# Kernel tuning notes

Measured on AMD Instinct MI355X. Metric: run time of the kernel, lower is better.

## Reference

```python
import jax, jax.numpy as jnp
import numpy as np

B, P, C, WIN = 64, 24, 40, 64          # batch, acoustic params, phoneme classes, window
L1 = WIN - 4                            # after conv k=5: 60
L2 = L1 - 4                             # after primary conv k=5: 56
R = P * L2                              # num_routes = 24*56 = 1344
IC, OC = 32, 16                         # capsule in/out channels
NUM_ITERS = 3


def squash(x, axis=-1):
    sq = jnp.sum(x * x, axis=axis, keepdims=True)
    return (sq / (1.0 + sq)) * x / (jnp.sqrt(sq) + 1e-8)


def conv1d(x, w, b):
    # x: (B, Cin, L), w: (Cout, Cin, K)
    out = jax.lax.conv_general_dilated(x, w, (1,), 'VALID',
                                       dimension_numbers=('NCH', 'OIH', 'NCH'))
    return out + b[None, :, None]


def batchnorm(x, g, b):
    # training-mode BN over (batch, length) per channel; x: (B, Ch, L)
    m = jnp.mean(x, axis=(0, 2), keepdims=True)
    v = jnp.var(x, axis=(0, 2), keepdims=True)
    return g[None, :, None] * (x - m) / jnp.sqrt(v + 1e-5) + b[None, :, None]


def setup_inputs() -> dict:
    key = jax.random.key(0)
    ks = jax.random.split(key, 12)
    d = {}
    d['x'] = jax.random.normal(ks[0], (B, WIN, P), dtype=jnp.float32)
    # project: Conv1d(24 -> 256, k=5) + BN(256)
    d['conv1_w'] = jax.random.normal(ks[1], (256, P, 5), dtype=jnp.float32) * (1.0 / np.sqrt(P * 5))
    d['conv1_b'] = jnp.zeros((256,), dtype=jnp.float32)
    d['bn1_g'] = jnp.ones((256,), dtype=jnp.float32)
    d['bn1_b'] = jnp.zeros((256,), dtype=jnp.float32)
    d['prim_w'] = jax.random.normal(ks[2], (P * 32, 256, 5), dtype=jnp.float32) * (1.0 / np.sqrt(256 * 5))
    d['prim_b'] = jnp.zeros((P * 32,), dtype=jnp.float32)
    d['bn2_g'] = jnp.ones((32,), dtype=jnp.float32)
    d['bn2_b'] = jnp.zeros((32,), dtype=jnp.float32)
    # digit capsule routing weights (1, C, R, 16, 32) as in torch (randn)
    d['W_cap'] = jax.random.normal(ks[3], (1, C, R, OC, IC), dtype=jnp.float32) * 0.05
    # classifier: Linear(16*C -> 256), Linear(256 -> C)
    d['cls_w1'] = jax.random.normal(ks[4], (256, OC * C), dtype=jnp.float32) * (1.0 / np.sqrt(OC * C))
    d['cls_b1'] = jnp.zeros((256,), dtype=jnp.float32)
    d['cls_w2'] = jax.random.normal(ks[5], (C, 256), dtype=jnp.float32) * (1.0 / np.sqrt(256))
    d['cls_b2'] = jnp.zeros((C,), dtype=jnp.float32)
    d['dec_w1'] = jax.random.normal(ks[6], (256, OC * C), dtype=jnp.float32) * (1.0 / np.sqrt(OC * C))
    d['dec_b1'] = jnp.zeros((256,), dtype=jnp.float32)
    d['dec_w2'] = jax.random.normal(ks[7], (WIN * P, 256), dtype=jnp.float32) * (1.0 / np.sqrt(256))
    d['dec_b2'] = jnp.zeros((WIN * P,), dtype=jnp.float32)
    return d


def reference(x, conv1_w, conv1_b, bn1_g, bn1_b, prim_w, prim_b, bn2_g, bn2_b,
              W_cap, cls_w1, cls_b1, cls_w2, cls_b2, dec_w1, dec_b1, dec_w2, dec_b2):
    h = jax.nn.relu(batchnorm(conv1d(jnp.transpose(x, (0, 2, 1)), conv1_w, conv1_b), bn1_g, bn1_b))
    # primary capsules: fused conv -> (B, 24*32, 56); capsule i occupies length slice i
    u = conv1d(h, prim_w, prim_b)                       # (B, 768, 56)
    u = u.reshape(B, P, 32, L2).transpose(0, 2, 1, 3).reshape(B, 32, R)  # concat along length dim
    u = batchnorm(u, bn2_g, bn2_b)
    u = squash(jnp.transpose(u, (0, 2, 1)), axis=-1)    # (B, R, 32)
    # digit capsule: u_hat = W @ x  -> (B, C, R, 16)
    u_hat = jnp.einsum('crdi,bri->bcrd', W_cap[0], u)
    # dynamic routing
    b_ij = jnp.zeros((B, C, R, 1), dtype=u_hat.dtype)
    for it in range(NUM_ITERS):
        c_ij = jax.nn.softmax(b_ij, axis=1)             # softmax over capsules
        s_j = jnp.sum(c_ij * u_hat, axis=2)             # (B, C, 16)
        v_j = squash(s_j, axis=-1)
        if it < NUM_ITERS - 1:
            a_ij = jnp.einsum('bcrd,bcd->bcr', u_hat, v_j)[..., None]
            b_ij = b_ij + a_ij
    flat = v_j.reshape(B, -1)                           # (B, 640)
    logits = jax.nn.relu(flat @ cls_w1.T + cls_b1) @ cls_w2.T + cls_b2
    pred_y = jax.nn.softmax(logits, axis=-1)
    # y is None branch: one-hot of argmax
    y = jax.nn.one_hot(jnp.argmax(pred_y, axis=1), C, dtype=v_j.dtype)
    masked = (v_j * y[:, :, None]).reshape(B, -1)
    pred_x = jax.nn.sigmoid(jax.nn.relu(masked @ dec_w1.T + dec_b1) @ dec_w2.T + dec_b2)
    pred_x = pred_x.reshape(B, WIN, P)
    return (pred_x, pred_y)
```

## Files before the change

### kernel.cpp

```cpp
#include <hip/hip_runtime.h>
#include <math.h>

#define BB_ 64
#define P_  24
#define C_  40
#define WIN_ 64
#define L1_ 60
#define L2_ 56
#define R_  1344

#define O_USQ   0ull
#define O_UHAT  2752512ull
#define O_H     30277632ull
#define O_HB    3735552ull
#define O_WT    4227072ull
#define O_UP    25755648ull
#define O_HID   31260672ull
#define O_HD    31277056ull
#define O_STATS 57802752ull
#define O_A1    57803328ull
#define O_B1S   57803584ull
#define O_A2    57803840ull
#define O_B2S   57803872ull
#define O_S     57803904ull
#define O_V     57967744ull
#define WS_FLOATS_NEEDED 58008704ull

typedef short bf16x8 __attribute__((ext_vector_type(8)));
typedef float f32x4 __attribute__((ext_vector_type(4)));

__device__ __forceinline__ float dot4f(float4 a, float4 b) {
    return a.x*b.x + a.y*b.y + a.z*b.z + a.w*b.w;
}

__device__ __forceinline__ unsigned short f2bf(float x) {
    unsigned int u = __float_as_uint(x);
    u += 0x7fffu + ((u >> 16) & 1u);
    return (unsigned short)(u >> 16);
}
__device__ __forceinline__ float bfl(unsigned int u) {
    return __uint_as_float(u << 16);
}
__device__ __forceinline__ float bfh(unsigned int u) {
    return __uint_as_float(u & 0xffff0000u);
}

__global__ void k0w(const float* __restrict__ w2, unsigned short* __restrict__ wt) {
    int o2 = blockIdx.x, t = threadIdx.x;
    const float* src = &w2[(size_t)o2 * 1280 + t * 5];
    #pragma unroll
    for (int kt = 0; kt < 5; kt++)
        wt[((size_t)kt * 768 + o2) * 256 + t] = f2bf(src[kt]);
}

__global__ void k1_conv1(const float* __restrict__ x, const float* __restrict__ w1,
                         const float* __restrict__ c1b, float* __restrict__ h) {
    __shared__ float xs[24 * 20];
    __shared__ float wl[64 * 121];
    int t = threadIdx.x;
    int lq = blockIdx.x, b = blockIdx.y, ocg = blockIdx.z;
    for (int idx = t; idx < 456; idx += 256) {
        int p = idx / 19, tau = idx - p * 19;
        xs[p * 20 + tau] = x[b * 1536 + (lq * 15 + tau) * 24 + p];
    }
    for (int idx = t; idx < 7680; idx += 256) {
        int o_ = idx / 120, cix = idx - o_ * 120;
        wl[o_ * 121 + cix] = w1[(ocg * 64 + o_) * 120 + cix];
    }
    __syncthreads();
    int g = t >> 6;
    int ol = t & 63;
    int LV = (g < 3) ? 4 : 3;
    int o = ocg * 64 + ol;
    float acc[4] = {0.f, 0.f, 0.f, 0.f};
    for (int p = 0; p < 24; p++) {
        float4 xa = *(const float4*)&xs[p * 20 + g * 4];
        float4 xb = *(const float4*)&xs[p * 20 + g * 4 + 4];
        float xr[8] = {xa.x, xa.y, xa.z, xa.w, xb.x, xb.y, xb.z, xb.w};
        #pragma unroll
        for (int k = 0; k < 5; k++) {
            float w = wl[ol * 121 + p * 5 + k];
            #pragma unroll
            for (int li = 0; li < 4; li++) acc[li] += xr[li + k] * w;
        }
    }
    for (int li = 0; li < LV; li++) {
        int l = lq * 15 + g * 4 + li;
        h[(size_t)(b * 60 + l) * 256 + o] = acc[li] + c1b[o];
    }
}

__global__ void k2a(const float* __restrict__ h, float* __restrict__ sum1, float* __restrict__ ss1) {
    int t = threadIdx.x;
    float s = 0.f, q = 0.f;
    for (int i = 0; i < 64; i++) {
        float v = h[(size_t)(blockIdx.x * 64 + i) * 256 + t];
        s += v; q += v * v;
    }
    atomicAdd(&sum1[t], s);
    atomicAdd(&ss1[t], q);
}

__global__ void k2b(const float* __restrict__ sum1, const float* __restrict__ ss1,
                    const float* __restrict__ g, const float* __restrict__ be,
                    float* __restrict__ a1, float* __restrict__ b1s) {
    int o = threadIdx.x;
    float m = sum1[o] * (1.f / 3840.f);
    float v = ss1[o] * (1.f / 3840.f) - m * m;
    float a = g[o] / sqrtf(v + 1e-5f);
    a1[o] = a;
    b1s[o] = be[o] - m * a;
}

__global__ void k2c(const float* __restrict__ h, const float* __restrict__ a1,
                    const float* __restrict__ b1s, unsigned short* __restrict__ hb) {
    int gid = blockIdx.x * 256 + threadIdx.x;
    int base = gid * 4;
    int ic = base & 255;
    float4 v = *(const float4*)&h[base];
    float4 a = *(const float4*)&a1[ic];
    float4 bb = *(const float4*)&b1s[ic];
    unsigned int w0 = (unsigned int)f2bf(fmaxf(v.x * a.x + bb.x, 0.f))
                    | ((unsigned int)f2bf(fmaxf(v.y * a.y + bb.y, 0.f)) << 16);
    unsigned int w1 = (unsigned int)f2bf(fmaxf(v.z * a.z + bb.z, 0.f))
                    | ((unsigned int)f2bf(fmaxf(v.w * a.w + bb.w, 0.f)) << 16);
    uint2 o = {w0, w1};
    *(uint2*)&hb[base] = o;
}

__global__ __launch_bounds__(256) void k3_mfma(
        const unsigned short* __restrict__ hb, const unsigned short* __restrict__ wt,
        const float* __restrict__ pb, float* __restrict__ up) {
    __shared__ unsigned short hs[68 * 40];
    __shared__ unsigned short wsd[5 * 64 * 40];
    int t = threadIdx.x;
    int m0 = blockIdx.x * 64;
    int b = blockIdx.y;
    int wid = t >> 6, lane = t & 63;
    int wm = wid >> 1, wn = wid & 1;
    int ln = lane & 15, grp = lane >> 4;

    f32x4 acc[2][2];
    #pragma unroll
    for (int i = 0; i < 2; i++)
        #pragma unroll
        for (int j = 0; j < 2; j++) acc[i][j] = (f32x4){0.f, 0.f, 0.f, 0.f};

    for (int ic0 = 0; ic0 < 256; ic0 += 32) {
        __syncthreads();
        for (int idx = t; idx < 272; idx += 256) {
            int row = idx >> 2, q = idx & 3;
            int hrow = row < 60 ? row : 59;
            uint4 v = *(const uint4*)&hb[((size_t)b * 60 + hrow) * 256 + ic0 + q * 8];
            *(uint4*)&hs[row * 40 + q * 8] = v;
        }
        #pragma unroll
        for (int it = 0; it < 5; it++) {
            int idx = it * 256 + t;
            int row = idx >> 2, q = idx & 3;
            int kt = row >> 6, o2l = row & 63;
            uint4 v = *(const uint4*)&wt[((size_t)kt * 768 + m0 + o2l) * 256 + ic0 + q * 8];
            *(uint4*)&wsd[row * 40 + q * 8] = v;
        }
        __syncthreads();
        #pragma unroll
        for (int kt = 0; kt < 5; kt++) {
            bf16x8 af0 = *(const bf16x8*)&wsd[(kt * 64 + wm * 32 + ln) * 40 + grp * 8];
            bf16x8 af1 = *(const bf16x8*)&wsd[(kt * 64 + wm * 32 + 16 + ln) * 40 + grp * 8];
            bf16x8 bf0 = *(const bf16x8*)&hs[(wn * 32 + ln + kt) * 40 + grp * 8];
            bf16x8 bf1 = *(const bf16x8*)&hs[(wn * 32 + 16 + ln + kt) * 40 + grp * 8];
            acc[0][0] = __builtin_amdgcn_mfma_f32_16x16x32_bf16(af0, bf0, acc[0][0], 0, 0, 0);
            acc[0][1] = __builtin_amdgcn_mfma_f32_16x16x32_bf16(af0, bf1, acc[0][1], 0, 0, 0);
            acc[1][0] = __builtin_amdgcn_mfma_f32_16x16x32_bf16(af1, bf0, acc[1][0], 0, 0, 0);
            acc[1][1] = __builtin_amdgcn_mfma_f32_16x16x32_bf16(af1, bf1, acc[1][1], 0, 0, 0);
        }
    }
    #pragma unroll
    for (int ms = 0; ms < 2; ms++) {
        int o2 = m0 + wm * 32 + ms * 16 + grp * 4;
        float4 pv = *(const float4*)&pb[o2];
        #pragma unroll
        for (int ns = 0; ns < 2; ns++) {
            int l = wn * 32 + ns * 16 + ln;
            if (l < 56) {
                float4 v;
                v.x = acc[ms][ns][0] + pv.x;
                v.y = acc[ms][ns][1] + pv.y;
                v.z = acc[ms][ns][2] + pv.z;
                v.w = acc[ms][ns][3] + pv.w;
                *(float4*)&up[(size_t)b * 43008 + (size_t)l * 768 + o2] = v;
            }
        }
    }
}

__global__ void k4s(const float* __restrict__ up, float* __restrict__ sum2, float* __restrict__ ss2) {
    __shared__ float rs[256], rq[256];
    int t = threadIdx.x;
    float s = 0.f, q = 0.f;
    for (int i = 0; i < 32; i++) {
        size_t row = (size_t)(blockIdx.x * 32 + i) * 768;
        for (int c0 = 0; c0 < 768; c0 += 256) {
            float v = up[row + c0 + t];
            s += v; q += v * v;
        }
    }
    rs[t] = s; rq[t] = q;
    __syncthreads();
    if (t < 32) {
        float S = 0.f, Q = 0.f;
        for (int g2 = 0; g2 < 8; g2++) { S += rs[t + 32 * g2]; Q += rq[t + 32 * g2]; }
        atomicAdd(&sum2[t], S);
        atomicAdd(&ss2[t], Q);
    }
}

__global__ void k4b(const float* __restrict__ sum2, const float* __restrict__ ss2,
                    const float* __restrict__ g, const float* __restrict__ be,
                    float* __restrict__ a2, float* __restrict__ b2s) {
    int j = threadIdx.x;
    if (j >= 32) return;
    float m = sum2[j] * (1.f / 86016.f);
    float v = ss2[j] * (1.f / 86016.f) - m * m;
    float a = g[j] / sqrtf(v + 1e-5f);
    a2[j] = a;
    b2s[j] = be[j] - m * a;
}

__global__ void k5(const float* __restrict__ up, const float* __restrict__ a2,
                   const float* __restrict__ b2s, float* __restrict__ usq) {
    int t = threadIdx.x;
    int row = blockIdx.x * 8 + (t >> 5);
    int j = t & 31;
    int b = row / 1344, r = row - b * 1344;
    int p = r / 56, l = r - p * 56;
    float v = up[(size_t)b * 43008 + (size_t)l * 768 + p * 32 + j];
    float xv = a2[j] * v + b2s[j];
    float sq = xv * xv;
    #pragma unroll
    for (int m = 16; m >= 1; m >>= 1) sq += __shfl_xor(sq, m, 32);
    float scale = (sq / (1.f + sq)) / (sqrtf(sq) + 1e-8f);
    usq[(size_t)row * 32 + j] = xv * scale;
}

__global__ __launch_bounds__(256) void k6_mfma(const float* __restrict__ usq,
                                               const float* __restrict__ W,
                                               unsigned short* __restrict__ uhb) {
    __shared__ unsigned short ub[64 * 40];
    __shared__ unsigned short db[2][4 * 64 * 20];
    int t = threadIdx.x;
    int r = blockIdx.x;
    {
        int b = t >> 2, ch = t & 3;
        const float* src = &usq[((size_t)b * 1344 + r) * 32 + ch * 8];
        float4 v0 = *(const float4*)&src[0];
        float4 v1 = *(const float4*)&src[4];
        uint4 pk;
        pk.x = (unsigned)f2bf(v0.x) | ((unsigned)f2bf(v0.y) << 16);
        pk.y = (unsigned)f2bf(v0.z) | ((unsigned)f2bf(v0.w) << 16);
        pk.z = (unsigned)f2bf(v1.x) | ((unsigned)f2bf(v1.y) << 16);
        pk.w = (unsigned)f2bf(v1.z) | ((unsigned)f2bf(v1.w) << 16);
        *(uint4*)&ub[b * 40 + ch * 8] = pk;
    }
    __syncthreads();
    int w = t >> 6, lane = t & 63;
    int ln = lane & 15, g = lane >> 4;
    bf16x8 bfr[4];
    #pragma unroll
    for (int nt = 0; nt < 4; nt++)
        bfr[nt] = *(const bf16x8*)&ub[(nt * 16 + ln) * 40 + g * 8];

    const float* abase = &W[((size_t)w * 1344 + r) * 512 + (size_t)ln * 32 + g * 8];
    float4 c0 = *(const float4*)&abase[0];
    float4 c1 = *(const float4*)&abase[4];
    for (int j = 0; j < 10; j++) {
        float4 n0, n1;
        if (j < 9) {
            const float* nsrc = abase + (size_t)(j + 1) * 4 * 688128ull;
            n0 = *(const float4*)&nsrc[0];
            n1 = *(const float4*)&nsrc[4];
        }
        union { bf16x8 v; unsigned int u[4]; } af;
        af.u[0] = (unsigned)f2bf(c0.x) | ((unsigned)f2bf(c0.y) << 16);
        af.u[1] = (unsigned)f2bf(c0.z) | ((unsigned)f2bf(c0.w) << 16);
        af.u[2] = (unsigned)f2bf(c1.x) | ((unsigned)f2bf(c1.y) << 16);
        af.u[3] = (unsigned)f2bf(c1.z) | ((unsigned)f2bf(c1.w) << 16);
        unsigned short* dbj = db[j & 1];
        #pragma unroll
        for (int nt = 0; nt < 4; nt++) {
            f32x4 acc = (f32x4){0.f, 0.f, 0.f, 0.f};
            acc = __builtin_amdgcn_mfma_f32_16x16x32_bf16(af.v, bfr[nt], acc, 0, 0, 0);
            int b = nt * 16 + ln;
            unsigned lo = (unsigned)f2bf(acc[0]) | ((unsigned)f2bf(acc[1]) << 16);
            unsigned hi = (unsigned)f2bf(acc[2]) | ((unsigned)f2bf(acc[3]) << 16);
            uint2 o = {lo, hi};
            *(uint2*)&dbj[(w * 64 + b) * 20 + g * 4] = o;
        }
        __syncthreads();
        {
            int b2 = t >> 2, q = t & 3;
            const unsigned short* srcl = &dbj[(q * 64 + b2) * 20];
            uint4 x0 = *(const uint4*)&srcl[0];
            uint4 x1 = *(const uint4*)&srcl[8];
            unsigned short* dst = &uhb[(((size_t)b2 * 1344 + r) * 40 + j * 4 + q) * 16];
            *(uint4*)&dst[0] = x0;
            *(uint4*)&dst[8] = x1;
        }
        c0 = n0; c1 = n1;
    }
}

template<int UNIFORM>
__global__ void k_route(const unsigned short* __restrict__ uhb, const float* __restrict__ vsum,
                        float* __restrict__ spart) {
    __shared__ float sl[2560];
    int t = threadIdx.x, wid = t >> 6, lane = t & 63;
    int b = blockIdx.y, rt = blockIdx.x;
    bool act = lane < 40;
    int c = act ? lane : 0;
    float4 vs0 = {0,0,0,0}, vs1 = vs0, vs2 = vs0, vs3 = vs0;
    if (UNIFORM == 0 && act) {
        const float4* vp = (const float4*)&vsum[b * 640 + c * 16];
        vs0 = vp[0]; vs1 = vp[1]; vs2 = vp[2]; vs3 = vp[3];
    }
    float4 ac0 = {0,0,0,0}, ac1 = ac0, ac2 = ac0, ac3 = ac0;
    for (int i = 0; i < 8; i++) {
        int r = rt * 32 + wid * 8 + i;
        const uint4* u4 = (const uint4*)&uhb[((size_t)(b * 1344 + r) * 40 + c) * 16];
        float4 a0 = {0,0,0,0}, a1 = a0, a2 = a0, a3 = a0;
        if (act) {
            uint4 q0 = u4[0], q1 = u4[1];
            a0.x = bfl(q0.x); a0.y = bfh(q0.x); a0.z = bfl(q0.y); a0.w = bfh(q0.y);
            a1.x = bfl(q0.z); a1.y = bfh(q0.z); a1.z = bfl(q0.w); a1.w = bfh(q0.w);
            a2.x = bfl(q1.x); a2.y = bfh(q1.x); a2.z = bfl(q1.y); a2.w = bfh(q1.y);
            a3.x = bfl(q1.z); a3.y = bfh(q1.z); a3.z = bfl(q1.w); a3.w = bfh(q1.w);
        }
        float w;
        if (UNIFORM) {
            w = 0.025f;
        } else {
            float dt = act ? (dot4f(a0, vs0) + dot4f(a1, vs1) + dot4f(a2, vs2) + dot4f(a3, vs3))
                           : -1e30f;
            float mx = dt;
            #pragma unroll
            for (int m2 = 32; m2 >= 1; m2 >>= 1) mx = fmaxf(mx, __shfl_xor(mx, m2));
            float e = act ? __expf(dt - mx) : 0.f;
            float se = e;
            #pragma unroll
            for (int m2 = 32; m2 >= 1; m2 >>= 1) se += __shfl_xor(se, m2);
            w = e / se;
        }
        ac0.x += w * a0.x; ac0.y += w * a0.y; ac0.z += w * a0.z; ac0.w += w * a0.w;
        ac1.x += w * a1.x; ac1.y += w * a1.y; ac1.z += w * a1.z; ac1.w += w * a1.w;
        ac2.x += w * a2.x; ac2.y += w * a2.y; ac2.z += w * a2.z; ac2.w += w * a2.w;
        ac3.x += w * a3.x; ac3.y += w * a3.y; ac3.z += w * a3.z; ac3.w += w * a3.w;
    }
    if (act) {
        float4* sp = (float4*)&sl[wid * 640 + c * 16];
        sp[0] = ac0; sp[1] = ac1; sp[2] = ac2; sp[3] = ac3;
    }
    __syncthreads();
    float* dst = spart + ((size_t)rt * 64 + b) * 640;
    for (int jj = t; jj < 640; jj += 256)
        dst[jj] = sl[jj] + sl[640 + jj] + sl[1280 + jj] + sl[1920 + jj];
}

__global__ void k8(const float* __restrict__ sp, float* __restrict__ vout,
                   float* __restrict__ vsum, int addsum) {
    int t = threadIdx.x;
    int row = blockIdx.x * 16 + (t >> 4);
    int d = t & 15;
    int b = row / 40, c = row - b * 40;
    const float* p = sp + (size_t)b * 640 + c * 16 + d;
    float v = 0.f;
    #pragma unroll 6
    for (int rt = 0; rt < 42; rt++) v += p[(size_t)rt * 40960];
    float sq = v * v;
    #pragma unroll
    for (int m = 8; m >= 1; m >>= 1) sq += __shfl_xor(sq, m, 16);
    float scale = (sq / (1.f + sq)) / (sqrtf(sq) + 1e-8f);
    float o = v * scale;
    vout[row * 16 + d] = o;
    if (addsum) vsum[row * 16 + d] += o;
}

__global__ void k10a(const float* __restrict__ v, const float* __restrict__ cw1,
                     const float* __restrict__ cb1, float* __restrict__ hid) {
    __shared__ float flat[640];
    int t = threadIdx.x;
    int b = blockIdx.x, hq = blockIdx.y;
    for (int j = t; j < 640; j += 256) flat[j] = v[b * 640 + j];
    __syncthreads();
    int h_l = t >> 2, s = t & 3;
    int h = hq * 64 + h_l;
    const float4* wr = (const float4*)&cw1[(size_t)h * 640 + s * 160];
    float a = 0.f;
    #pragma unroll
    for (int u = 0; u < 40; u++) {
        float4 w4 = wr[u];
        float4 f4 = *(const float4*)&flat[s * 160 + u * 4];
        a += dot4f(w4, f4);
    }
    a += __shfl_xor(a, 1);
    a += __shfl_xor(a, 2);
    if (s == 0) hid[b * 256 + h] = fmaxf(a + cb1[h], 0.f);
}

__global__ void k10bc(const float* __restrict__ v, const float* __restrict__ hid,
                      const float* __restrict__ cw2, const float* __restrict__ cb2,
                      const float* __restrict__ dw1, const float* __restrict__ db1,
                      float* __restrict__ out, float* __restrict__ hd) {
    __shared__ float hl[256], lgs[40], msk[16];
    __shared__ float smx, ssum;
    __shared__ int chat;
    int t = threadIdx.x, b = blockIdx.x;
    if (t < 256) hl[t] = hid[b * 256 + t];
    __syncthreads();
    {
        int c = t >> 3, s = t & 7;
        float p = 0.f;
        const float4* w4 = (const float4*)&cw2[c * 256 + s * 32];
        const float4* h4 = (const float4*)&hl[s * 32];
        #pragma unroll
        for (int u = 0; u < 8; u++) p += dot4f(w4[u], h4[u]);
        p += __shfl_xor(p, 1); p += __shfl_xor(p, 2); p += __shfl_xor(p, 4);
        if (s == 0) lgs[c] = p + cb2[c];
    }
    __syncthreads();
    if (t == 0) {
        float mx = lgs[0]; int am = 0;
        for (int c2 = 1; c2 < 40; c2++) if (lgs[c2] > mx) { mx = lgs[c2]; am = c2; }
        float se = 0.f;
        for (int c2 = 0; c2 < 40; c2++) se += __expf(lgs[c2] - mx);
        smx = mx; ssum = se; chat = am;
    }
    __syncthreads();
    if (t < 40) out[98304 + b * 40 + t] = __expf(lgs[t] - smx) / ssum;
    if (t < 16) msk[t] = v[b * 640 + chat * 16 + t];
    __syncthreads();
    if (t < 256) {
        int cb = chat * 16;
        float ad = db1[t];
        const float4* w4 = (const float4*)&dw1[(size_t)t * 640 + cb];
        #pragma unroll
        for (int u = 0; u < 4; u++) {
            float4 m4 = *(const float4*)&msk[u * 4];
            ad += dot4f(w4[u], m4);
        }
        hd[b * 256 + t] = fmaxf(ad, 0.f);
    }
}

__global__ void k10d(const float* __restrict__ hd, const float* __restrict__ dw2,
                     const float* __restrict__ db2, float* __restrict__ out) {
    __shared__ float hl[256];
    int t = threadIdx.x;
    int b = blockIdx.x, ot = blockIdx.y;
    if (t < 256) hl[t] = hd[b * 256 + t];
    __syncthreads();
    int o_l = t >> 2, s = t & 3;
    int o = ot * 64 + o_l;
    const float4* w4 = (const float4*)&dw2[(size_t)o * 256 + s * 64];
    const float4* h4 = (const float4*)&hl[s * 64];
    float z = 0.f;
    #pragma unroll
    for (int u = 0; u < 16; u++) z += dot4f(w4[u], h4[u]);
    z += __shfl_xor(z, 1);
    z += __shfl_xor(z, 2);
    if (s == 0) out[b * 1536 + o] = 1.f / (1.f + __expf(-(z + db2[o])));
}

extern "C" void kernel_launch(void* const* d_in, const int* in_sizes, int n_in,
                              void* d_out, int out_size, void* d_ws, size_t ws_size,
                              hipStream_t stream) {
    const float* x   = (const float*)d_in[0];
    const float* c1w = (const float*)d_in[1];
    const float* c1b = (const float*)d_in[2];
    const float* g1  = (const float*)d_in[3];
    const float* be1 = (const float*)d_in[4];
    const float* pw  = (const float*)d_in[5];
    const float* pb  = (const float*)d_in[6];
    const float* g2  = (const float*)d_in[7];
    const float* be2 = (const float*)d_in[8];
    const float* Wc  = (const float*)d_in[9];
    const float* cw1 = (const float*)d_in[10];
    const float* cb1 = (const float*)d_in[11];
    const float* cw2 = (const float*)d_in[12];
    const float* cb2 = (const float*)d_in[13];
    const float* dw1 = (const float*)d_in[14];
    const float* db1 = (const float*)d_in[15];
    const float* dw2 = (const float*)d_in[16];
    const float* db2 = (const float*)d_in[17];

    if (ws_size < WS_FLOATS_NEEDED * 4ull) return;

    float* ws  = (float*)d_ws;
    float* out = (float*)d_out;
    float* usq  = ws + O_USQ;
    float* spart = ws + O_USQ;
    unsigned short* uhb = (unsigned short*)(ws + O_UHAT);
    float* hpre = ws + O_H;
    unsigned short* hbb = (unsigned short*)(ws + O_HB);
    unsigned short* wtb = (unsigned short*)(ws + O_WT);
    float* up   = ws + O_UP;
    float* hidb = ws + O_HID;
    float* hdb  = ws + O_HD;
    float* sum1 = ws + O_STATS;
    float* ss1  = sum1 + 256;
    float* sum2 = ss1 + 256;
    float* ss2  = sum2 + 32;
    float* a1  = ws + O_A1;
    float* b1s = ws + O_B1S;
    float* a2  = ws + O_A2;
    float* b2s = ws + O_B2S;
    float* vsum = ws + O_S;
    float* vbuf = ws + O_V;

    hipMemsetAsync(sum1, 0, 576 * sizeof(float), stream);
    hipMemsetAsync(vsum, 0, 40960 * sizeof(float), stream);

    k0w<<<768, 256, 0, stream>>>(pw, wtb);
    k1_conv1<<<dim3(4, 64, 4), 256, 0, stream>>>(x, c1w, c1b, hpre);
    k2a<<<60, 256, 0, stream>>>(hpre, sum1, ss1);
    k2b<<<1, 256, 0, stream>>>(sum1, ss1, g1, be1, a1, b1s);
    k2c<<<960, 256, 0, stream>>>(hpre, a1, b1s, hbb);
    k3_mfma<<<dim3(12, 64), 256, 0, stream>>>(hbb, wtb, pb, up);
    k4s<<<112, 256, 0, stream>>>(up, sum2, ss2);
    k4b<<<1, 64, 0, stream>>>(sum2, ss2, g2, be2, a2, b2s);
    k5<<<10752, 256, 0, stream>>>(up, a2, b2s, usq);
    k6_mfma<<<1344, 256, 0, stream>>>(usq, Wc, uhb);
    k_route<1><<<dim3(42, 64), 256, 0, stream>>>(uhb, nullptr, spart);
    k8<<<160, 256, 0, stream>>>(spart, vbuf, vsum, 1);
    k_route<0><<<dim3(42, 64), 256, 0, stream>>>(uhb, vsum, spart);
    k8<<<160, 256, 0, stream>>>(spart, vbuf, vsum, 1);
    k_route<0><<<dim3(42, 64), 256, 0, stream>>>(uhb, vsum, spart);
    k8<<<160, 256, 0, stream>>>(spart, vbuf, vsum, 0);
    k10a<<<dim3(64, 4), 256, 0, stream>>>(vbuf, cw1, cb1, hidb);
    k10bc<<<64, 320, 0, stream>>>(vbuf, hidb, cw2, cb2, dw1, db1, out, hdb);
    k10d<<<dim3(64, 24), 256, 0, stream>>>(hdb, dw2, db2, out);
}
```

Measured before the change: 388.5 us.

## Restructure capsule projection and routing kernels around shared-memory tiles

The u_hat projection kernel now runs with 128 threads per block. Each wave handles 20 capsule classes, prefetching four class tiles at a time, and stages its output per wave so it can write contiguous 1280-byte rows without block-wide barriers. The routing kernel first loads a whole 32-route tile of u_hat into shared memory with coalesced 16-byte loads. It then computes per-route softmax weights with 8 threads per route, and does a weighted reduction in which 160 threads each accumulate over the 32 routes. This replaces the old per-wave scattered loads, the 40-of-64 active lanes and the full-wave shuffle softmax, at the cost of more shared memory and a serial 32-step loop.

```diff
diff --git a/kernel.cpp b/kernel.cpp
--- a/kernel.cpp
+++ b/kernel.cpp
@@ -38,6 +38,9 @@
     u += 0x7fffu + ((u >> 16) & 1u);
     return (unsigned short)(u >> 16);
 }
+__device__ __forceinline__ unsigned int pk2(float a, float b) {
+    return (unsigned int)f2bf(a) | ((unsigned int)f2bf(b) << 16);
+}
 __device__ __forceinline__ float bfl(unsigned int u) {
     return __uint_as_float(u << 16);
 }
@@ -120,10 +123,8 @@
     float4 v = *(const float4*)&h[base];
     float4 a = *(const float4*)&a1[ic];
     float4 bb = *(const float4*)&b1s[ic];
-    unsigned int w0 = (unsigned int)f2bf(fmaxf(v.x * a.x + bb.x, 0.f))
-                    | ((unsigned int)f2bf(fmaxf(v.y * a.y + bb.y, 0.f)) << 16);
-    unsigned int w1 = (unsigned int)f2bf(fmaxf(v.z * a.z + bb.z, 0.f))
-                    | ((unsigned int)f2bf(fmaxf(v.w * a.w + bb.w, 0.f)) << 16);
+    unsigned int w0 = pk2(fmaxf(v.x * a.x + bb.x, 0.f), fmaxf(v.y * a.y + bb.y, 0.f));
+    unsigned int w1 = pk2(fmaxf(v.z * a.z + bb.z, 0.f), fmaxf(v.w * a.w + bb.w, 0.f));
     uint2 o = {w0, w1};
     *(uint2*)&hb[base] = o;
 }
@@ -243,24 +244,24 @@
     usq[(size_t)row * 32 + j] = xv * scale;
 }
 
-__global__ __launch_bounds__(256) void k6_mfma(const float* __restrict__ usq,
+__global__ __launch_bounds__(128) void k6_mfma(const float* __restrict__ usq,
                                                const float* __restrict__ W,
                                                unsigned short* __restrict__ uhb) {
     __shared__ unsigned short ub[64 * 40];
-    __shared__ unsigned short db[2][4 * 64 * 20];
+    __shared__ unsigned short dpk[2][64 * 72];
     int t = threadIdx.x;
     int r = blockIdx.x;
     {
-        int b = t >> 2, ch = t & 3;
-        const float* src = &usq[((size_t)b * 1344 + r) * 32 + ch * 8];
+        int b = t >> 1, hf = t & 1;
+        const float* src = &usq[((size_t)b * 1344 + r) * 32 + hf * 16];
         float4 v0 = *(const float4*)&src[0];
         float4 v1 = *(const float4*)&src[4];
-        uint4 pk;
-        pk.x = (unsigned)f2bf(v0.x) | ((unsigned)f2bf(v0.y) << 16);
-        pk.y = (unsigned)f2bf(v0.z) | ((unsigned)f2bf(v0.w) << 16);
-        pk.z = (unsigned)f2bf(v1.x) | ((unsigned)f2bf(v1.y) << 16);
-        pk.w = (unsigned)f2bf(v1.z) | ((unsigned)f2bf(v1.w) << 16);
-        *(uint4*)&ub[b * 40 + ch * 8] = pk;
+        float4 v2 = *(const float4*)&src[8];
+        float4 v3 = *(const float4*)&src[12];
+        uint4 p0 = {pk2(v0.x, v0.y), pk2(v0.z, v0.w), pk2(v1.x, v1.y), pk2(v1.z, v1.w)};
+        uint4 p1 = {pk2(v2.x, v2.y), pk2(v2.z, v2.w), pk2(v3.x, v3.y), pk2(v3.z, v3.w)};
+        *(uint4*)&ub[b * 40 + hf * 16] = p0;
+        *(uint4*)&ub[b * 40 + hf * 16 + 8] = p1;
     }
     __syncthreads();
     int w = t >> 6, lane = t & 63;
@@ -270,99 +271,117 @@
     for (int nt = 0; nt < 4; nt++)
         bfr[nt] = *(const bf16x8*)&ub[(nt * 16 + ln) * 40 + g * 8];
 
-    const float* abase = &W[((size_t)w * 1344 + r) * 512 + (size_t)ln * 32 + g * 8];
-    float4 c0 = *(const float4*)&abase[0];
-    float4 c1 = *(const float4*)&abase[4];
-    for (int j = 0; j < 10; j++) {
-        float4 n0, n1;
-        if (j < 9) {
-            const float* nsrc = abase + (size_t)(j + 1) * 4 * 688128ull;
-            n0 = *(const float4*)&nsrc[0];
-            n1 = *(const float4*)&nsrc[4];
-        }
-        union { bf16x8 v; unsigned int u[4]; } af;
-        af.u[0] = (unsigned)f2bf(c0.x) | ((unsigned)f2bf(c0.y) << 16);
-        af.u[1] = (unsigned)f2bf(c0.z) | ((unsigned)f2bf(c0.w) << 16);
-        af.u[2] = (unsigned)f2bf(c1.x) | ((unsigned)f2bf(c1.y) << 16);
-        af.u[3] = (unsigned)f2bf(c1.z) | ((unsigned)f2bf(c1.w) << 16);
-        unsigned short* dbj = db[j & 1];
-        #pragma unroll
-        for (int nt = 0; nt < 4; nt++) {
-            f32x4 acc = (f32x4){0.f, 0.f, 0.f, 0.f};
-            acc = __builtin_amdgcn_mfma_f32_16x16x32_bf16(af.v, bfr[nt], acc, 0, 0, 0);
-            int b = nt * 16 + ln;
-            unsigned lo = (unsigned)f2bf(acc[0]) | ((unsigned)f2bf(acc[1]) << 16);
-            unsigned hi = (unsigned)f2bf(acc[2]) | ((unsigned)f2bf(acc[3]) << 16);
-            uint2 o = {lo, hi};
-            *(uint2*)&dbj[(w * 64 + b) * 20 + g * 4] = o;
-        }
+    unsigned short* dw = dpk[w];
+    float4 pa[4][2], na[4][2];
+    #pragma unroll
+    for (int cl = 0; cl < 4; cl++) {
+        const float* s = &W[(((size_t)(w * 20 + cl) * 1344 + r) * 16 + ln) * 32 + g * 8];
+        pa[cl][0] = *(const float4*)&s[0];
+        pa[cl][1] = *(const float4*)&s[4];
+    }
+    #pragma unroll
+    for (int k = 0; k < 5; k++) {
+        int qd = w * 5 + k;
+        if (k < 4) {
+            #pragma unroll
+            for (int cl = 0; cl < 4; cl++) {
+                const float* s = &W[(((size_t)((qd + 1) * 4 + cl) * 1344 + r) * 16 + ln) * 32 + g * 8];
+                na[cl][0] = *(const float4*)&s[0];
+                na[cl][1] = *(const float4*)&s[4];
+            }
+        }
+        #pragma unroll
+        for (int cl = 0; cl < 4; cl++) {
+            union { bf16x8 v; unsigned int u[4]; } af;
+            af.u[0] = pk2(pa[cl][0].x, pa[cl][0].y);
+            af.u[1] = pk2(pa[cl][0].z, pa[cl][0].w);
+            af.u[2] = pk2(pa[cl][1].x, pa[cl][1].y);
+            af.u[3] = pk2(pa[cl][1].z, pa[cl][1].w);
+            #pragma unroll
+            for (int nt = 0; nt < 4; nt++) {
+                f32x4 acc = (f32x4){0.f, 0.f, 0.f, 0.f};
+                acc = __builtin_amdgcn_mfma_f32_16x16x32_bf16(af.v, bfr[nt], acc, 0, 0, 0);
+                int b = nt * 16 + ln;
+                uint2 o = {pk2(acc[0], acc[1]), pk2(acc[2], acc[3])};
+                *(uint2*)&dw[b * 72 + cl * 16 + g * 4] = o;
+            }
+        }
+        {
+            const uint4* row = (const uint4*)&dw[lane * 72];
+            unsigned short* dst = &uhb[(((size_t)lane * 1344 + r) * 40 + qd * 4) * 16];
+            #pragma unroll
+            for (int kk = 0; kk < 8; kk++)
+                *(uint4*)&dst[kk * 8] = row[kk];
+        }
+        #pragma unroll
+        for (int cl = 0; cl < 4; cl++) { pa[cl][0] = na[cl][0]; pa[cl][1] = na[cl][1]; }
+    }
+}
+
+template<int UNIFORM>
+__global__ __launch_bounds__(256) void k_route(const unsigned short* __restrict__ uhb,
+                                               const float* __restrict__ vsum,
+                                               float* __restrict__ spart) {
+    __shared__ unsigned short tile[32 * 83 * 8];
+    __shared__ float wl[32 * 42];
+    __shared__ float vl[640];
+    int t = threadIdx.x;
+    int b = blockIdx.y, rt = blockIdx.x;
+    const uint4* gsrc = (const uint4*)&uhb[(size_t)(b * 1344 + rt * 32) * 640];
+    uint4* t16 = (uint4*)tile;
+    #pragma unroll
+    for (int k = 0; k < 10; k++) {
+        int ch = k * 256 + t;
+        int rl = ch / 80, q = ch - rl * 80;
+        t16[rl * 83 + q] = gsrc[ch];
+    }
+    if (UNIFORM == 0) {
+        if (t < 160) ((float4*)vl)[t] = ((const float4*)&vsum[b * 640])[t];
+    }
+    __syncthreads();
+    if (UNIFORM == 0) {
+        int rl = t >> 3, oct = t & 7;
+        float dts[5];
+        #pragma unroll
+        for (int cc = 0; cc < 5; cc++) {
+            int c = oct * 5 + cc;
+            uint4 q0 = t16[rl * 83 + c * 2];
+            uint4 q1 = t16[rl * 83 + c * 2 + 1];
+            const float4* v4 = (const float4*)&vl[c * 16];
+            float4 w0 = v4[0], w1 = v4[1], w2 = v4[2], w3 = v4[3];
+            dts[cc] = bfl(q0.x)*w0.x + bfh(q0.x)*w0.y + bfl(q0.y)*w0.z + bfh(q0.y)*w0.w
+                    + bfl(q0.z)*w1.x + bfh(q0.z)*w1.y + bfl(q0.w)*w1.z + bfh(q0.w)*w1.w
+                    + bfl(q1.x)*w2.x + bfh(q1.x)*w2.y + bfl(q1.y)*w2.z + bfh(q1.y)*w2.w
+                    + bfl(q1.z)*w3.x + bfh(q1.z)*w3.y + bfl(q1.w)*w3.z + bfh(q1.w)*w3.w;
+        }
+        float mx = fmaxf(fmaxf(fmaxf(dts[0], dts[1]), fmaxf(dts[2], dts[3])), dts[4]);
+        mx = fmaxf(mx, __shfl_xor(mx, 1));
+        mx = fmaxf(mx, __shfl_xor(mx, 2));
+        mx = fmaxf(mx, __shfl_xor(mx, 4));
+        float es[5], ps = 0.f;
+        #pragma unroll
+        for (int cc = 0; cc < 5; cc++) { es[cc] = __expf(dts[cc] - mx); ps += es[cc]; }
+        ps += __shfl_xor(ps, 1);
+        ps += __shfl_xor(ps, 2);
+        ps += __shfl_xor(ps, 4);
+        float inv = 1.f / ps;
+        #pragma unroll
+        for (int cc = 0; cc < 5; cc++) wl[rl * 42 + oct * 5 + cc] = es[cc] * inv;
         __syncthreads();
-        {
-            int b2 = t >> 2, q = t & 3;
-            const unsigned short* srcl = &dbj[(q * 64 + b2) * 20];
-            uint4 x0 = *(const uint4*)&srcl[0];
-            uint4 x1 = *(const uint4*)&srcl[8];
-            unsigned short* dst = &uhb[(((size_t)b2 * 1344 + r) * 40 + j * 4 + q) * 16];
-            *(uint4*)&dst[0] = x0;
-            *(uint4*)&dst[8] = x1;
-        }
-        c0 = n0; c1 = n1;
-    }
-}
-
-template<int UNIFORM>
-__global__ void k_route(const unsigned short* __restrict__ uhb, const float* __restrict__ vsum,
-                        float* __restrict__ spart) {
-    __shared__ float sl[2560];
-    int t = threadIdx.x, wid = t >> 6, lane = t & 63;
-    int b = blockIdx.y, rt = blockIdx.x;
-    bool act = lane < 40;
-    int c = act ? lane : 0;
-    float4 vs0 = {0,0,0,0}, vs1 = vs0, vs2 = vs0, vs3 = vs0;
-    if (UNIFORM == 0 && act) {
-        const float4* vp = (const float4*)&vsum[b * 640 + c * 16];
-        vs0 = vp[0]; vs1 = vp[1]; vs2 = vp[2]; vs3 = vp[3];
-    }
-    float4 ac0 = {0,0,0,0}, ac1 = ac0, ac2 = ac0, ac3 = ac0;
-    for (int i = 0; i < 8; i++) {
-        int r = rt * 32 + wid * 8 + i;
-        const uint4* u4 = (const uint4*)&uhb[((size_t)(b * 1344 + r) * 40 + c) * 16];
-        float4 a0 = {0,0,0,0}, a1 = a0, a2 = a0, a3 = a0;
-        if (act) {
-            uint4 q0 = u4[0], q1 = u4[1];
-            a0.x = bfl(q0.x); a0.y = bfh(q0.x); a0.z = bfl(q0.y); a0.w = bfh(q0.y);
-            a1.x = bfl(q0.z); a1.y = bfh(q0.z); a1.z = bfl(q0.w); a1.w = bfh(q0.w);
-            a2.x = bfl(q1.x); a2.y = bfh(q1.x); a2.z = bfl(q1.y); a2.w = bfh(q1.y);
-            a3.x = bfl(q1.z); a3.y = bfh(q1.z); a3.z = bfl(q1.w); a3.w = bfh(q1.w);
-        }
-        float w;
-        if (UNIFORM) {
-            w = 0.025f;
-        } else {
-            float dt = act ? (dot4f(a0, vs0) + dot4f(a1, vs1) + dot4f(a2, vs2) + dot4f(a3, vs3))
-                           : -1e30f;
-            float mx = dt;
-            #pragma unroll
-            for (int m2 = 32; m2 >= 1; m2 >>= 1) mx = fmaxf(mx, __shfl_xor(mx, m2));
-            float e = act ? __expf(dt - mx) : 0.f;
-            float se = e;
-            #pragma unroll
-            for (int m2 = 32; m2 >= 1; m2 >>= 1) se += __shfl_xor(se, m2);
-            w = e / se;
-        }
-        ac0.x += w * a0.x; ac0.y += w * a0.y; ac0.z += w * a0.z; ac0.w += w * a0.w;
-        ac1.x += w * a1.x; ac1.y += w * a1.y; ac1.z += w * a1.z; ac1.w += w * a1.w;
-        ac2.x += w * a2.x; ac2.y += w * a2.y; ac2.z += w * a2.z; ac2.w += w * a2.w;
-        ac3.x += w * a3.x; ac3.y += w * a3.y; ac3.z += w * a3.z; ac3.w += w * a3.w;
-    }
-    if (act) {
-        float4* sp = (float4*)&sl[wid * 640 + c * 16];
-        sp[0] = ac0; sp[1] = ac1; sp[2] = ac2; sp[3] = ac3;
-    }
-    __syncthreads();
-    float* dst = spart + ((size_t)rt * 64 + b) * 640;
-    for (int jj = t; jj < 640; jj += 256)
-        dst[jj] = sl[jj] + sl[640 + jj] + sl[1280 + jj] + sl[1920 + jj];
+    }
+    if (t < 160) {
+        int c = t >> 2, dq = t & 3;
+        float a0 = 0.f, a1 = 0.f, a2 = 0.f, a3 = 0.f;
+        const uint2* t8 = (const uint2*)tile;
+        for (int rl = 0; rl < 32; rl++) {
+            float wv = UNIFORM ? 0.025f : wl[rl * 42 + c];
+            uint2 u = t8[(rl * 83 + c * 2) * 2 + dq];
+            a0 += wv * bfl(u.x); a1 += wv * bfh(u.x);
+            a2 += wv * bfl(u.y); a3 += wv * bfh(u.y);
+        }
+        float4 o = {a0, a1, a2, a3};
+        *(float4*)&spart[((size_t)rt * 64 + b) * 640 + c * 16 + dq * 4] = o;
+    }
 }
 
 __global__ void k8(const float* __restrict__ sp, float* __restrict__ vout,
@@ -528,7 +547,7 @@
     k4s<<<112, 256, 0, stream>>>(up, sum2, ss2);
     k4b<<<1, 64, 0, stream>>>(sum2, ss2, g2, be2, a2, b2s);
     k5<<<10752, 256, 0, stream>>>(up, a2, b2s, usq);
-    k6_mfma<<<1344, 256, 0, stream>>>(usq, Wc, uhb);
+    k6_mfma<<<1344, 128, 0, stream>>>(usq, Wc, uhb);
     k_route<1><<<dim3(42, 64), 256, 0, stream>>>(uhb, nullptr, spart);
     k8<<<160, 256, 0, stream>>>(spart, vbuf, vsum, 1);
     k_route<0><<<dim3(42, 64), 256, 0, stream>>>(uhb, vsum, spart);
```

New measurement: 427.4 us. 1.1x slower.

## Fuse BN2+squash into u_hat kernel and make u_hat route-major

Applied to the files above, without the earlier changes.

Removes the separate k5 kernel that applied batchnorm and squash and wrote usq. k6_mfma now reads the primary conv output directly, applies BN and squash in registers with a 4-lane shuffle reduction, and packs the result to bf16. This drops one launch and a full fp32 write-and-read pass. The u_hat buffer layout changes from (b, r) to (r, b) ordering, so k6 writes contiguously per route block and k_route reads with the matching index. The up buffer is moved to a new workspace offset so it no longer overlaps the region it previously shared.

```diff
diff --git a/kernel.cpp b/kernel.cpp
--- a/kernel.cpp
+++ b/kernel.cpp
@@ -14,9 +14,9 @@
 #define O_H     30277632ull
 #define O_HB    3735552ull
 #define O_WT    4227072ull
-#define O_UP    25755648ull
 #define O_HID   31260672ull
 #define O_HD    31277056ull
+#define O_UP    31293440ull
 #define O_STATS 57802752ull
 #define O_A1    57803328ull
 #define O_B1S   57803584ull
@@ -37,6 +37,9 @@
     unsigned int u = __float_as_uint(x);
     u += 0x7fffu + ((u >> 16) & 1u);
     return (unsigned short)(u >> 16);
+}
+__device__ __forceinline__ unsigned int pk2(float a, float b) {
+    return (unsigned int)f2bf(a) | ((unsigned int)f2bf(b) << 16);
 }
 __device__ __forceinline__ float bfl(unsigned int u) {
     return __uint_as_float(u << 16);
@@ -120,10 +123,8 @@
     float4 v = *(const float4*)&h[base];
     float4 a = *(const float4*)&a1[ic];
     float4 bb = *(const float4*)&b1s[ic];
-    unsigned int w0 = (unsigned int)f2bf(fmaxf(v.x * a.x + bb.x, 0.f))
-                    | ((unsigned int)f2bf(fmaxf(v.y * a.y + bb.y, 0.f)) << 16);
-    unsigned int w1 = (unsigned int)f2bf(fmaxf(v.z * a.z + bb.z, 0.f))
-                    | ((unsigned int)f2bf(fmaxf(v.w * a.w + bb.w, 0.f)) << 16);
+    unsigned int w0 = pk2(fmaxf(v.x * a.x + bb.x, 0.f), fmaxf(v.y * a.y + bb.y, 0.f));
+    unsigned int w1 = pk2(fmaxf(v.z * a.z + bb.z, 0.f), fmaxf(v.w * a.w + bb.w, 0.f));
     uint2 o = {w0, w1};
     *(uint2*)&hb[base] = o;
 }
@@ -227,39 +228,34 @@
     b2s[j] = be[j] - m * a;
 }
 
-__global__ void k5(const float* __restrict__ up, const float* __restrict__ a2,
-                   const float* __restrict__ b2s, float* __restrict__ usq) {
-    int t = threadIdx.x;
-    int row = blockIdx.x * 8 + (t >> 5);
-    int j = t & 31;
-    int b = row / 1344, r = row - b * 1344;
-    int p = r / 56, l = r - p * 56;
-    float v = up[(size_t)b * 43008 + (size_t)l * 768 + p * 32 + j];
-    float xv = a2[j] * v + b2s[j];
-    float sq = xv * xv;
-    #pragma unroll
-    for (int m = 16; m >= 1; m >>= 1) sq += __shfl_xor(sq, m, 32);
-    float scale = (sq / (1.f + sq)) / (sqrtf(sq) + 1e-8f);
-    usq[(size_t)row * 32 + j] = xv * scale;
-}
-
-__global__ __launch_bounds__(256) void k6_mfma(const float* __restrict__ usq,
+__global__ __launch_bounds__(256) void k6_mfma(const float* __restrict__ up,
+                                               const float* __restrict__ a2v,
+                                               const float* __restrict__ b2v,
                                                const float* __restrict__ W,
                                                unsigned short* __restrict__ uhb) {
     __shared__ unsigned short ub[64 * 40];
     __shared__ unsigned short db[2][4 * 64 * 20];
     int t = threadIdx.x;
     int r = blockIdx.x;
+    int p = r / 56, l = r - p * 56;
     {
         int b = t >> 2, ch = t & 3;
-        const float* src = &usq[((size_t)b * 1344 + r) * 32 + ch * 8];
+        int j0 = ch * 8;
+        const float* src = &up[(size_t)b * 43008 + (size_t)l * 768 + p * 32 + j0];
         float4 v0 = *(const float4*)&src[0];
         float4 v1 = *(const float4*)&src[4];
-        uint4 pk;
-        pk.x = (unsigned)f2bf(v0.x) | ((unsigned)f2bf(v0.y) << 16);
-        pk.y = (unsigned)f2bf(v0.z) | ((unsigned)f2bf(v0.w) << 16);
-        pk.z = (unsigned)f2bf(v1.x) | ((unsigned)f2bf(v1.y) << 16);
-        pk.w = (unsigned)f2bf(v1.z) | ((unsigned)f2bf(v1.w) << 16);
+        float xs[8] = {v0.x, v0.y, v0.z, v0.w, v1.x, v1.y, v1.z, v1.w};
+        float sq = 0.f;
+        #pragma unroll
+        for (int k2 = 0; k2 < 8; k2++) {
+            xs[k2] = a2v[j0 + k2] * xs[k2] + b2v[j0 + k2];
+            sq += xs[k2] * xs[k2];
+        }
+        sq += __shfl_xor(sq, 1);
+        sq += __shfl_xor(sq, 2);
+        float scale = (sq / (1.f + sq)) / (sqrtf(sq) + 1e-8f);
+        uint4 pk = {pk2(xs[0]*scale, xs[1]*scale), pk2(xs[2]*scale, xs[3]*scale),
+                    pk2(xs[4]*scale, xs[5]*scale), pk2(xs[6]*scale, xs[7]*scale)};
         *(uint4*)&ub[b * 40 + ch * 8] = pk;
     }
     __syncthreads();
@@ -281,19 +277,17 @@
             n1 = *(const float4*)&nsrc[4];
         }
         union { bf16x8 v; unsigned int u[4]; } af;
-        af.u[0] = (unsigned)f2bf(c0.x) | ((unsigned)f2bf(c0.y) << 16);
-        af.u[1] = (unsigned)f2bf(c0.z) | ((unsigned)f2bf(c0.w) << 16);
-        af.u[2] = (unsigned)f2bf(c1.x) | ((unsigned)f2bf(c1.y) << 16);
-        af.u[3] = (unsigned)f2bf(c1.z) | ((unsigned)f2bf(c1.w) << 16);
+        af.u[0] = pk2(c0.x, c0.y);
+        af.u[1] = pk2(c0.z, c0.w);
+        af.u[2] = pk2(c1.x, c1.y);
+        af.u[3] = pk2(c1.z, c1.w);
         unsigned short* dbj = db[j & 1];
         #pragma unroll
         for (int nt = 0; nt < 4; nt++) {
             f32x4 acc = (f32x4){0.f, 0.f, 0.f, 0.f};
             acc = __builtin_amdgcn_mfma_f32_16x16x32_bf16(af.v, bfr[nt], acc, 0, 0, 0);
             int b = nt * 16 + ln;
-            unsigned lo = (unsigned)f2bf(acc[0]) | ((unsigned)f2bf(acc[1]) << 16);
-            unsigned hi = (unsigned)f2bf(acc[2]) | ((unsigned)f2bf(acc[3]) << 16);
-            uint2 o = {lo, hi};
+            uint2 o = {pk2(acc[0], acc[1]), pk2(acc[2], acc[3])};
             *(uint2*)&dbj[(w * 64 + b) * 20 + g * 4] = o;
         }
         __syncthreads();
@@ -302,7 +296,7 @@
             const unsigned short* srcl = &dbj[(q * 64 + b2) * 20];
             uint4 x0 = *(const uint4*)&srcl[0];
             uint4 x1 = *(const uint4*)&srcl[8];
-            unsigned short* dst = &uhb[(((size_t)b2 * 1344 + r) * 40 + j * 4 + q) * 16];
+            unsigned short* dst = &uhb[((size_t)r * 64 + b2) * 640 + (size_t)(j * 4 + q) * 16];
             *(uint4*)&dst[0] = x0;
             *(uint4*)&dst[8] = x1;
         }
@@ -326,7 +320,7 @@
     float4 ac0 = {0,0,0,0}, ac1 = ac0, ac2 = ac0, ac3 = ac0;
     for (int i = 0; i < 8; i++) {
         int r = rt * 32 + wid * 8 + i;
-        const uint4* u4 = (const uint4*)&uhb[((size_t)(b * 1344 + r) * 40 + c) * 16];
+        const uint4* u4 = (const uint4*)&uhb[((size_t)(r * 64 + b) * 40 + c) * 16];
         float4 a0 = {0,0,0,0}, a1 = a0, a2 = a0, a3 = a0;
         if (act) {
             uint4 q0 = u4[0], q1 = u4[1];
@@ -496,7 +490,6 @@
 
     float* ws  = (float*)d_ws;
     float* out = (float*)d_out;
-    float* usq  = ws + O_USQ;
     float* spart = ws + O_USQ;
     unsigned short* uhb = (unsigned short*)(ws + O_UHAT);
     float* hpre = ws + O_H;
@@ -527,8 +520,7 @@
     k3_mfma<<<dim3(12, 64), 256, 0, stream>>>(hbb, wtb, pb, up);
     k4s<<<112, 256, 0, stream>>>(up, sum2, ss2);
     k4b<<<1, 64, 0, stream>>>(sum2, ss2, g2, be2, a2, b2s);
-    k5<<<10752, 256, 0, stream>>>(up, a2, b2s, usq);
-    k6_mfma<<<1344, 256, 0, stream>>>(usq, Wc, uhb);
+    k6_mfma<<<1344, 256, 0, stream>>>(up, a2, b2s, Wc, uhb);
     k_route<1><<<dim3(42, 64), 256, 0, stream>>>(uhb, nullptr, spart);
     k8<<<160, 256, 0, stream>>>(spart, vbuf, vsum, 1);
     k_route<0><<<dim3(42, 64), 256, 0, stream>>>(uhb, vsum, spart);
```

Result: no change. 384.6 us (-1.0%).
